# Performance work log

Measured on AMD Instinct MI355X. Metric: run time of the kernel, lower is better.

Reference implementation:

```python
import jax, jax.numpy as jnp
import numpy as np

EMB = 1024
HEADS = 16
SCALE = (EMB // HEADS) ** (-0.5)


def setup_inputs() -> dict:
    key = jax.random.key(0)
    k1, k2, k3, k4, k5 = jax.random.split(key, 5)
    x = jax.random.normal(k1, (2, 2048, EMB), dtype=jnp.float32)
    w_qkv = jax.random.normal(k2, (EMB, 3 * EMB), dtype=jnp.float32) * (EMB ** -0.5)
    b_qkv = jax.random.normal(k3, (3 * EMB,), dtype=jnp.float32) * 0.02
    w_proj = jax.random.normal(k4, (EMB, EMB), dtype=jnp.float32) * (EMB ** -0.5)
    b_proj = jax.random.normal(k5, (EMB,), dtype=jnp.float32) * 0.02
    return {"x": x, "w_qkv": w_qkv, "b_qkv": b_qkv, "w_proj": w_proj, "b_proj": b_proj}


def reference(x, w_qkv, b_qkv, w_proj, b_proj):
    b, n, d = x.shape
    # qkv projection; split last dim as (heads, head_dim, 3) exactly like the
    # torch reshape, then permute to (3, b, h, n, head_dim)
    qkv = (x @ w_qkv + b_qkv).reshape(b, n, HEADS, -1, 3)
    qkv = jnp.transpose(qkv, (4, 0, 2, 1, 3))
    q, k, v = qkv[0], qkv[1], qkv[2]
    energy = jnp.einsum('bhqd,bhkd->bhqk', q, k)  # full n x n scores
    att = jax.nn.softmax(energy, axis=-1) * SCALE  # softmax THEN scale (as in source)
    out = jnp.einsum('bhqk,bhkd->bhqd', att, v)
    out = jnp.transpose(out, (0, 2, 1, 3)).reshape(b, n, d)
    return out @ w_proj + b_proj
```

## Files before the change

kernel.cpp:

```cpp
#include <hip/hip_runtime.h>
#include <cstdint>

#define SEQ   2048
#define BATCH 2
#define EMB   1024
#define NH    16
#define HD    64
#define MROWS (BATCH*SEQ)
#define NQKV  (3*EMB)
#define SCALE 0.125f
#define L2E   1.4426950408889634f

typedef _Float16 half8 __attribute__((ext_vector_type(8)));
typedef _Float16 half4 __attribute__((ext_vector_type(4)));
typedef __fp16   fp16x2 __attribute__((ext_vector_type(2)));
typedef float    floatx4 __attribute__((ext_vector_type(4)));

#define MFMA(a,b,c) __builtin_amdgcn_mfma_f32_16x16x32_f16(a, b, c, 0, 0, 0)

__device__ __forceinline__ void async16(const void* g, const void* l) {
    __builtin_amdgcn_global_load_lds(
        (const __attribute__((address_space(1))) unsigned int*)(uintptr_t)g,
        (__attribute__((address_space(3))) unsigned int*)(uint32_t)(uintptr_t)l,
        16, 0, 0);
}

__global__ void k_split(const float* __restrict__ src, _Float16* __restrict__ hi, int n4) {
    int i = blockIdx.x * blockDim.x + threadIdx.x;
    if (i >= n4) return;
    float4 v = ((const float4*)src)[i];
    half4 h;
    h[0] = (_Float16)v.x;
    h[1] = (_Float16)v.y;
    h[2] = (_Float16)v.z;
    h[3] = (_Float16)v.w;
    ((half4*)hi)[i] = h;
}

__global__ void k_transpose_split(const float* __restrict__ w, _Float16* __restrict__ hi,
                                  int K, int N) {
    __shared__ float t[32][33];
    int n0 = blockIdx.x * 32, k0 = blockIdx.y * 32;
    int tx = threadIdx.x, ty = threadIdx.y;
    #pragma unroll
    for (int i = 0; i < 4; i++)
        t[ty + i * 8][tx] = w[(size_t)(k0 + ty + i * 8) * N + n0 + tx];
    __syncthreads();
    #pragma unroll
    for (int i = 0; i < 4; i++) {
        float v = t[tx][ty + i * 8];
        hi[(size_t)(n0 + ty + i * 8) * K + k0 + tx] = (_Float16)v;
    }
}

template<int MODE, int NT>
__global__ __launch_bounds__(256, 2)
void k_gemm(const _Float16* __restrict__ A, const _Float16* __restrict__ Bt,
            const float* __restrict__ bias,
            _Float16* __restrict__ outQ, _Float16* __restrict__ outK,
            _Float16* __restrict__ outV, float* __restrict__ outC,
            int Mdim, int Ndim, int Kdim) {
    constexpr int WN  = NT / 2;
    constexpr int NTI = WN / 16;
    constexpr int LB  = NT / 64;
    __shared__ _Float16 smem[2][(128 + NT) * 32];

    const int tid = threadIdx.x;
    const int lane = tid & 63, wid = tid >> 6;
    const int quad = lane >> 4, l16 = lane & 15;
    const int wm = (wid >> 1) * 64, wn = (wid & 1) * WN;
    const int m0 = blockIdx.y * 128, n0 = blockIdx.x * NT;

    const int row4 = tid >> 2, slot4 = tid & 3;

    auto stage = [&](int k0, int buf) {
        _Float16* As = smem[buf];
        _Float16* Bs = smem[buf] + 128 * 32;
        #pragma unroll
        for (int i = 0; i < 2; i++) {
            int c = i * 256 + tid;
            int row = i * 64 + row4;
            int q = slot4 ^ ((row >> 1) & 3);
            async16(A + (size_t)(m0 + row) * Kdim + k0 + q * 8, As + c * 8);
        }
        #pragma unroll
        for (int i = 0; i < LB; i++) {
            int c = i * 256 + tid;
            int row = i * 64 + row4;
            int q = slot4 ^ ((row >> 1) & 3);
            async16(Bt + (size_t)(n0 + row) * Kdim + k0 + q * 8, Bs + c * 8);
        }
    };

    floatx4 acc[4][NTI];
    #pragma unroll
    for (int i = 0; i < 4; i++)
        #pragma unroll
        for (int j = 0; j < NTI; j++)
            acc[i][j] = (floatx4){0.f, 0.f, 0.f, 0.f};

    const int NIT = Kdim >> 5;
    stage(0, 0);

    for (int it = 0; it < NIT; it++) {
        const int p = it & 1;
        const int k0n = ((it + 1 == NIT) ? 0 : (it + 1)) << 5;
        stage(k0n, p ^ 1);
        if constexpr (LB == 2) asm volatile("s_waitcnt vmcnt(4)" ::: "memory");
        else                   asm volatile("s_waitcnt vmcnt(3)" ::: "memory");
        asm volatile("s_barrier" ::: "memory");

        const _Float16* As = smem[p];
        const _Float16* Bs = smem[p] + 128 * 32;
        half8 af[4], bf[NTI];
        #pragma unroll
        for (int t = 0; t < 4; t++) {
            int rowA = wm + t * 16 + l16;
            af[t] = *(const half8*)(As + rowA * 32 + (quad ^ ((rowA >> 1) & 3)) * 8);
        }
        #pragma unroll
        for (int t = 0; t < NTI; t++) {
            int rowB = wn + t * 16 + l16;
            bf[t] = *(const half8*)(Bs + rowB * 32 + (quad ^ ((rowB >> 1) & 3)) * 8);
        }
        #pragma unroll
        for (int mt = 0; mt < 4; mt++)
            #pragma unroll
            for (int nt = 0; nt < NTI; nt++)
                acc[mt][nt] = MFMA(af[mt], bf[nt], acc[mt][nt]);

        asm volatile("s_barrier" ::: "memory");
    }

    #pragma unroll
    for (int mt = 0; mt < 4; mt++) {
        int rowg = m0 + wm + mt * 16 + quad * 4;
        #pragma unroll
        for (int nt = 0; nt < NTI; nt++) {
            int colg = n0 + wn + nt * 16 + l16;
            float bv = bias[colg];
            if (MODE == 0) {
                int h = colg / 192, rem = colg % 192;
                int d = rem / 3, which = rem % 3;
                #pragma unroll
                for (int r = 0; r < 4; r++) {
                    int m = rowg + r;
                    int b = m >> 11, s = m & (SEQ - 1);
                    int bh = b * NH + h;
                    _Float16 hv = (_Float16)(acc[mt][nt][r] + bv);
                    if (which == 0)      outQ[((size_t)bh * SEQ + s) * HD + d] = hv;
                    else if (which == 1) outK[((size_t)bh * SEQ + s) * HD + d] = hv;
                    else                 outV[((size_t)bh * HD + d) * SEQ + s] = hv;
                }
            } else {
                #pragma unroll
                for (int r = 0; r < 4; r++)
                    outC[(size_t)(rowg + r) * Ndim + colg] = acc[mt][nt][r] + bv;
            }
        }
    }
}

__device__ __forceinline__ int swzK(int row) { return (row ^ (row >> 2)) & 7; }
__device__ __forceinline__ int swzV(int row) { return (row ^ (row >> 1)) & 7; }

__global__ __launch_bounds__(256, 2)
void k_attn(const _Float16* __restrict__ Q, const _Float16* __restrict__ K,
            const _Float16* __restrict__ Vt, _Float16* __restrict__ Aout) {
    __shared__ __align__(16) _Float16 Ks[2][128 * 64];
    __shared__ __align__(16) _Float16 Vs[2][80 * 128];

    const int tid = threadIdx.x;
    const int lane = tid & 63, wid = tid >> 6;
    const int quad = lane >> 4, l16 = lane & 15;

    const int n = blockIdx.x;
    const int bh = (n & 7) * 4 + (n >> 7);
    const int q0 = ((n >> 3) & 15) * 128;

    const _Float16* Qb = Q  + (size_t)bh * SEQ * HD;
    const _Float16* Kb = K  + (size_t)bh * SEQ * HD;
    const _Float16* Vb = Vt + (size_t)bh * HD * SEQ;

    const int rA = ((l16 >> 2) << 3) | (l16 & 3);
    const int grayl = (l16 ^ (l16 >> 1)) & 7;

    {
        half8 one8;
        #pragma unroll
        for (int r = 0; r < 8; r++) one8[r] = (_Float16)1.0f;
        ((half8*)(Vs[0] + 64 * 128))[tid] = one8;
        ((half8*)(Vs[1] + 64 * 128))[tid] = one8;
    }
    __syncthreads();

    half8 qf[2][2];
    #pragma unroll
    for (int qt = 0; qt < 2; qt++)
        #pragma unroll
        for (int kc = 0; kc < 2; kc++)
            qf[qt][kc] = *(const half8*)(Qb + (size_t)(q0 + wid * 32 + qt * 16 + l16) * HD
                                          + kc * 32 + quad * 8);

    #pragma unroll
    for (int i = 0; i < 4; i++) {
        int c = i * 256 + tid;
        int rowK = c >> 3, posK = c & 7;
        async16(Kb + (size_t)rowK * HD + (posK ^ swzK(rowK)) * 8, Ks[0] + c * 8);
        int rowV = c >> 4, posV = c & 15;
        int qv = (posV & 8) | ((posV & 7) ^ swzV(rowV));
        async16(Vb + (size_t)rowV * SEQ + qv * 8, Vs[0] + c * 8);
    }

    floatx4 o[2][4], o_l[2];
    float mi[2] = {-1e30f, -1e30f};
    #pragma unroll
    for (int qt = 0; qt < 2; qt++) {
        #pragma unroll
        for (int dt = 0; dt < 4; dt++) o[qt][dt] = (floatx4){0.f, 0.f, 0.f, 0.f};
        o_l[qt] = (floatx4){0.f, 0.f, 0.f, 0.f};
    }

    #pragma unroll 2
    for (int t = 0; t < 16; t++) {
        const int p = t & 1;
        const int kvn = ((t + 1) & 15) * 128;
        #pragma unroll
        for (int i = 0; i < 4; i++) {
            int c = i * 256 + tid;
            int rowK = c >> 3, posK = c & 7;
            async16(Kb + (size_t)(kvn + rowK) * HD + (posK ^ swzK(rowK)) * 8,
                    Ks[p ^ 1] + c * 8);
            int rowV = c >> 4, posV = c & 15;
            int qv = (posV & 8) | ((posV & 7) ^ swzV(rowV));
            async16(Vb + (size_t)rowV * SEQ + kvn + qv * 8, Vs[p ^ 1] + c * 8);
        }
        asm volatile("s_waitcnt vmcnt(8)" ::: "memory");
        asm volatile("s_barrier" ::: "memory");

        const _Float16* Ksp = Ks[p];
        const _Float16* Vsp = Vs[p];

        floatx4 sv[4][2][2];
        #pragma unroll
        for (int u = 0; u < 4; u++)
            #pragma unroll
            for (int e = 0; e < 2; e++) {
                int row = u * 32 + e * 4 + rA;
                int sw = swzK(row);
                const _Float16* base = Ksp + row * 64;
                half8 kf0 = *(const half8*)(base + ((quad ^ sw) << 3));
                half8 kf1 = *(const half8*)(base + (((quad + 4) ^ sw) << 3));
                floatx4 z = (floatx4){0.f, 0.f, 0.f, 0.f};
                #pragma unroll
                for (int qt = 0; qt < 2; qt++) {
                    floatx4 s = MFMA(kf0, qf[qt][0], z);
                    sv[u][e][qt] = MFMA(kf1, qf[qt][1], s);
                }
            }

        #pragma unroll
        for (int qt = 0; qt < 2; qt++) {
            float mb = -1e30f;
            #pragma unroll
            for (int u = 0; u < 4; u++)
                #pragma unroll
                for (int e = 0; e < 2; e++)
                    #pragma unroll
                    for (int r = 0; r < 4; r++)
                        mb = fmaxf(mb, sv[u][e][qt][r]);
            mb = fmaxf(mb, __shfl_xor(mb, 16));
            mb = fmaxf(mb, __shfl_xor(mb, 32));
            float Mn = fmaxf(mi[qt], mb * L2E);
            float al = __builtin_amdgcn_exp2f(mi[qt] - Mn);
            mi[qt] = Mn;
            float alq[4];
            #pragma unroll
            for (int r = 0; r < 4; r++)
                alq[r] = __shfl(al, quad * 4 + r);
            #pragma unroll
            for (int dt = 0; dt < 4; dt++)
                #pragma unroll
                for (int r = 0; r < 4; r++)
                    o[qt][dt][r] *= alq[r];
            #pragma unroll
            for (int r = 0; r < 4; r++)
                o_l[qt][r] *= alq[r];
        }

        #pragma unroll
        for (int u = 0; u < 4; u++) {
            half8 af[2];
            #pragma unroll
            for (int qt = 0; qt < 2; qt++) {
                float p0[8];
                #pragma unroll
                for (int r = 0; r < 4; r++) {
                    p0[r]     = __builtin_amdgcn_exp2f(fmaf(sv[u][0][qt][r], L2E, -mi[qt]));
                    p0[4 + r] = __builtin_amdgcn_exp2f(fmaf(sv[u][1][qt][r], L2E, -mi[qt]));
                }
                union { fp16x2 h2[4]; half8 v; } pk;
                pk.h2[0] = __builtin_amdgcn_cvt_pkrtz(p0[0], p0[1]);
                pk.h2[1] = __builtin_amdgcn_cvt_pkrtz(p0[2], p0[3]);
                pk.h2[2] = __builtin_amdgcn_cvt_pkrtz(p0[4], p0[5]);
                pk.h2[3] = __builtin_amdgcn_cvt_pkrtz(p0[6], p0[7]);
                af[qt] = pk.v;
            }
            int q = u * 4 + quad;
            int slotbase = (q & 8) | ((q & 7) ^ grayl);
            #pragma unroll
            for (int dt = 0; dt < 4; dt++) {
                int row = dt * 16 + l16;
                half8 vf = *(const half8*)(Vsp + row * 128 + slotbase * 8);
                o[0][dt] = MFMA(af[0], vf, o[0][dt]);
                o[1][dt] = MFMA(af[1], vf, o[1][dt]);
            }
            half8 vfl = *(const half8*)(Vsp + (64 + l16) * 128 + slotbase * 8);
            o_l[0] = MFMA(af[0], vfl, o_l[0]);
            o_l[1] = MFMA(af[1], vfl, o_l[1]);
        }

        asm volatile("s_barrier" ::: "memory");
    }

    int b = bh >> 4, h = bh & 15;
    #pragma unroll
    for (int qt = 0; qt < 2; qt++)
        #pragma unroll
        for (int r = 0; r < 4; r++) {
            float inv = SCALE / o_l[qt][r];
            int srow = q0 + wid * 32 + qt * 16 + quad * 4 + r;
            #pragma unroll
            for (int dt = 0; dt < 4; dt++) {
                int col = h * HD + dt * 16 + l16;
                Aout[(size_t)(b * SEQ + srow) * EMB + col] = (_Float16)(o[qt][dt][r] * inv);
            }
        }
}

extern "C" void kernel_launch(void* const* d_in, const int* in_sizes, int n_in,
                              void* d_out, int out_size, void* d_ws, size_t ws_size,
                              hipStream_t stream) {
    (void)in_sizes; (void)n_in; (void)out_size; (void)ws_size;
    const float* x      = (const float*)d_in[0];
    const float* w_qkv  = (const float*)d_in[1];
    const float* b_qkv  = (const float*)d_in[2];
    const float* w_proj = (const float*)d_in[3];
    const float* b_proj = (const float*)d_in[4];

    char* ws = (char*)d_ws;
    const size_t MB = 1ull << 20;
    _Float16* x_hi  = (_Float16*)(ws + 0 * MB);
    _Float16* wq_hi = (_Float16*)(ws + 8 * MB);
    _Float16* wp_hi = (_Float16*)(ws + 14 * MB);
    _Float16* Qb    = (_Float16*)(ws + 16 * MB);
    _Float16* Kb    = (_Float16*)(ws + 24 * MB);
    _Float16* Vtb   = (_Float16*)(ws + 32 * MB);
    _Float16* attb  = (_Float16*)(ws + 40 * MB);

    k_split<<<(MROWS * EMB / 4) / 256, 256, 0, stream>>>(x, x_hi, MROWS * EMB / 4);
    k_transpose_split<<<dim3(NQKV / 32, EMB / 32), dim3(32, 8), 0, stream>>>(
        w_qkv, wq_hi, EMB, NQKV);
    k_transpose_split<<<dim3(EMB / 32, EMB / 32), dim3(32, 8), 0, stream>>>(
        w_proj, wp_hi, EMB, EMB);
    k_gemm<0, 128><<<dim3(NQKV / 128, MROWS / 128), 256, 0, stream>>>(
        x_hi, wq_hi, b_qkv, Qb, Kb, Vtb, nullptr, MROWS, NQKV, EMB);
    k_attn<<<dim3(512), 256, 0, stream>>>(Qb, Kb, Vtb, attb);
    k_gemm<1, 64><<<dim3(EMB / 64, MROWS / 128), 256, 0, stream>>>(
        attb, wp_hi, b_proj, nullptr, nullptr, nullptr,
        (float*)d_out, MROWS, EMB, EMB);
}
```

Before: 201.9 us.

## Warp-specialize GEMM with dedicated producer waves for async LDS loads

Doubles the GEMM block to 512 threads, with four waves that only issue global-to-LDS async loads and four waves that only run MFMA math. The two groups hand off through paired barriers instead of each thread both loading and computing. The aim is to overlap memory traffic with compute without the compute waves stalling on vmcnt. The cost is extra waves that occupy slots and a barrier protocol that must match exactly. The launch bound of 4 blocks of 512 per CU may also limit register use or occupancy.

```diff
diff --git a/kernel.cpp b/kernel.cpp
--- a/kernel.cpp
+++ b/kernel.cpp
@@ -54,7 +54,7 @@
 }
 
 template<int MODE, int NT>
-__global__ __launch_bounds__(256, 2)
+__global__ __launch_bounds__(512, 4)
 void k_gemm(const _Float16* __restrict__ A, const _Float16* __restrict__ Bt,
             const float* __restrict__ bias,
             _Float16* __restrict__ outQ, _Float16* __restrict__ outK,
@@ -63,34 +63,49 @@
     constexpr int WN  = NT / 2;
     constexpr int NTI = WN / 16;
     constexpr int LB  = NT / 64;
-    __shared__ _Float16 smem[2][(128 + NT) * 32];
+    __shared__ _Float16 As[2][128 * 32];
+    __shared__ _Float16 Bs[2][NT * 32];
 
     const int tid = threadIdx.x;
-    const int lane = tid & 63, wid = tid >> 6;
+    const int wid = tid >> 6;
+    const int m0 = blockIdx.y * 128, n0 = blockIdx.x * NT;
+    const int NIT = Kdim >> 5;
+
+    if (wid >= 4) {
+        const int ptid = tid & 255;
+        const int prow = ptid >> 2, pslot = ptid & 3;
+        auto stage = [&](int k0, int buf) {
+            #pragma unroll
+            for (int i = 0; i < 2; i++) {
+                int c = i * 256 + ptid;
+                int row = i * 64 + prow;
+                int q = pslot ^ ((row >> 1) & 3);
+                async16(A + (size_t)(m0 + row) * Kdim + k0 + q * 8, As[buf] + c * 8);
+            }
+            #pragma unroll
+            for (int i = 0; i < LB; i++) {
+                int c = i * 256 + ptid;
+                int row = i * 64 + prow;
+                int q = pslot ^ ((row >> 1) & 3);
+                async16(Bt + (size_t)(n0 + row) * Kdim + k0 + q * 8, Bs[buf] + c * 8);
+            }
+        };
+        stage(0, 0);
+        for (int it = 0; it < NIT; it++) {
+            const int k0n = ((it + 1 == NIT) ? 0 : (it + 1)) << 5;
+            stage(k0n, (it & 1) ^ 1);
+            if constexpr (LB == 2) asm volatile("s_waitcnt vmcnt(4)" ::: "memory");
+            else                   asm volatile("s_waitcnt vmcnt(3)" ::: "memory");
+            asm volatile("s_barrier" ::: "memory");
+            asm volatile("s_barrier" ::: "memory");
+        }
+        asm volatile("s_waitcnt vmcnt(0)" ::: "memory");
+        return;
+    }
+
+    const int lane = tid & 63;
     const int quad = lane >> 4, l16 = lane & 15;
     const int wm = (wid >> 1) * 64, wn = (wid & 1) * WN;
-    const int m0 = blockIdx.y * 128, n0 = blockIdx.x * NT;
-
-    const int row4 = tid >> 2, slot4 = tid & 3;
-
-    auto stage = [&](int k0, int buf) {
-        _Float16* As = smem[buf];
-        _Float16* Bs = smem[buf] + 128 * 32;
-        #pragma unroll
-        for (int i = 0; i < 2; i++) {
-            int c = i * 256 + tid;
-            int row = i * 64 + row4;
-            int q = slot4 ^ ((row >> 1) & 3);
-            async16(A + (size_t)(m0 + row) * Kdim + k0 + q * 8, As + c * 8);
-        }
-        #pragma unroll
-        for (int i = 0; i < LB; i++) {
-            int c = i * 256 + tid;
-            int row = i * 64 + row4;
-            int q = slot4 ^ ((row >> 1) & 3);
-            async16(Bt + (size_t)(n0 + row) * Kdim + k0 + q * 8, Bs + c * 8);
-        }
-    };
 
     floatx4 acc[4][NTI];
     #pragma unroll
@@ -99,36 +114,25 @@
         for (int j = 0; j < NTI; j++)
             acc[i][j] = (floatx4){0.f, 0.f, 0.f, 0.f};
 
-    const int NIT = Kdim >> 5;
-    stage(0, 0);
-
     for (int it = 0; it < NIT; it++) {
+        asm volatile("s_barrier" ::: "memory");
         const int p = it & 1;
-        const int k0n = ((it + 1 == NIT) ? 0 : (it + 1)) << 5;
-        stage(k0n, p ^ 1);
-        if constexpr (LB == 2) asm volatile("s_waitcnt vmcnt(4)" ::: "memory");
-        else                   asm volatile("s_waitcnt vmcnt(3)" ::: "memory");
-        asm volatile("s_barrier" ::: "memory");
-
-        const _Float16* As = smem[p];
-        const _Float16* Bs = smem[p] + 128 * 32;
         half8 af[4], bf[NTI];
         #pragma unroll
         for (int t = 0; t < 4; t++) {
             int rowA = wm + t * 16 + l16;
-            af[t] = *(const half8*)(As + rowA * 32 + (quad ^ ((rowA >> 1) & 3)) * 8);
+            af[t] = *(const half8*)(As[p] + rowA * 32 + (quad ^ ((rowA >> 1) & 3)) * 8);
         }
         #pragma unroll
         for (int t = 0; t < NTI; t++) {
             int rowB = wn + t * 16 + l16;
-            bf[t] = *(const half8*)(Bs + rowB * 32 + (quad ^ ((rowB >> 1) & 3)) * 8);
+            bf[t] = *(const half8*)(Bs[p] + rowB * 32 + (quad ^ ((rowB >> 1) & 3)) * 8);
         }
         #pragma unroll
         for (int mt = 0; mt < 4; mt++)
             #pragma unroll
             for (int nt = 0; nt < NTI; nt++)
                 acc[mt][nt] = MFMA(af[mt], bf[nt], acc[mt][nt]);
-
         asm volatile("s_barrier" ::: "memory");
     }
 
@@ -363,10 +367,10 @@
         w_qkv, wq_hi, EMB, NQKV);
     k_transpose_split<<<dim3(EMB / 32, EMB / 32), dim3(32, 8), 0, stream>>>(
         w_proj, wp_hi, EMB, EMB);
-    k_gemm<0, 128><<<dim3(NQKV / 128, MROWS / 128), 256, 0, stream>>>(
+    k_gemm<0, 128><<<dim3(NQKV / 128, MROWS / 128), 512, 0, stream>>>(
         x_hi, wq_hi, b_qkv, Qb, Kb, Vtb, nullptr, MROWS, NQKV, EMB);
     k_attn<<<dim3(512), 256, 0, stream>>>(Qb, Kb, Vtb, attb);
-    k_gemm<1, 64><<<dim3(EMB / 64, MROWS / 128), 256, 0, stream>>>(
+    k_gemm<1, 64><<<dim3(EMB / 64, MROWS / 128), 512, 0, stream>>>(
         attb, wp_hi, b_proj, nullptr, nullptr, nullptr,
         (float*)d_out, MROWS, EMB, EMB);
 }
```

After: 204.9 us. No clear change (+1.5%).
